# Kernel optimization log

Hardware: AMD Instinct MI355X
Metric: run time of the kernel (lower is better)

## Reference

```python
import jax, jax.numpy as jnp
import numpy as np

QUERY_SIZE = 512
KEY_SIZE = 512
VALUE_SIZE = 512
HIDDEN = 128


def setup_inputs() -> dict:
    key = jax.random.key(0)
    ks = jax.random.split(key, 9)
    b, t_q, t_k = 8, 128, 512
    query = jax.random.normal(ks[0], (b, t_q, QUERY_SIZE), dtype=jnp.float32)
    keys = jax.random.normal(ks[1], (b, t_k, KEY_SIZE), dtype=jnp.float32)
    values = jax.random.normal(ks[2], (b, t_k, VALUE_SIZE), dtype=jnp.float32)
    # torch nn.Linear init ~ U(-1/sqrt(fan_in), 1/sqrt(fan_in)); scale-matched normals are fine
    sq = 1.0 / np.sqrt(QUERY_SIZE)
    sk = 1.0 / np.sqrt(KEY_SIZE)
    sh = 1.0 / np.sqrt(HIDDEN)
    Wq = jax.random.uniform(ks[3], (HIDDEN, QUERY_SIZE), jnp.float32, -sq, sq)
    bq = jax.random.uniform(ks[4], (HIDDEN,), jnp.float32, -sq, sq)
    Wk = jax.random.uniform(ks[5], (HIDDEN, KEY_SIZE), jnp.float32, -sk, sk)
    bk = jax.random.uniform(ks[6], (HIDDEN,), jnp.float32, -sk, sk)
    Wo = jax.random.uniform(ks[7], (1, HIDDEN), jnp.float32, -sh, sh)
    bo = jax.random.uniform(ks[8], (1,), jnp.float32, -sh, sh)
    return {"query": query, "keys": keys, "values": values,
            "Wq": Wq, "bq": bq, "Wk": Wk, "bk": bk, "Wo": Wo, "bo": bo}


def reference(query, keys, values, Wq, bq, Wk, bk, Wo, bo):
    # Bahdanau additive attention: att_ij = Wo @ tanh(Wq q_i + Wk k_j + bq + bk) + bo
    # Project once per position (mathematically identical to the expanded per-pair Linear).
    q_proj = jnp.einsum('bqn,hn->bqh', query, Wq) + bq          # b x t_q x h
    k_proj = jnp.einsum('bkn,hn->bkh', keys, Wk) + bk           # b x t_k x h
    hid = jnp.tanh(q_proj[:, :, None, :] + k_proj[:, None, :, :])  # b x t_q x t_k x h
    scores = jnp.einsum('bqkh,h->bqk', hid, Wo[0]) + bo[0]       # b x t_q x t_k
    attn = jax.nn.softmax(scores, axis=2)
    context = jnp.einsum('bqk,bkv->bqv', attn, values)           # b x t_q x n_v
    return context, attn
```

## Files before the change

### kernel.cpp

```cpp
#include <hip/hip_runtime.h>


#define B_    8
#define TQ_   128
#define TK_   512
#define NIN_  512
#define H_    128
#define NV_   512
#define NQR   (B_*TQ_)
#define NROWS (NQR + B_*TK_)
#define CTXN  (B_*TQ_*NV_)

#define C2_   2.8853900817779268f
#define L2E_  1.4426950408889634f

__device__ __forceinline__ float fexp2(float x){ return __builtin_amdgcn_exp2f(x); }
__device__ __forceinline__ float frcp (float x){ return __builtin_amdgcn_rcpf(x); }

__global__ __launch_bounds__(256, 5) void proj_kernel(
        const float* __restrict__ query, const float* __restrict__ keys,
        const float* __restrict__ Wq, const float* __restrict__ Wk,
        float* __restrict__ psum, int kper) {
    __shared__ float at[32][18];
    __shared__ float wt[32][132];
    const int tid = threadIdx.x;
    const int r0  = blockIdx.x * 16;
    const float* in; const float* W;
    if (r0 < NQR) { in = query + (size_t)r0 * NIN_;         W = Wq; }
    else          { in = keys  + (size_t)(r0 - NQR) * NIN_; W = Wk; }

    const int r2 = (tid >> 5) * 2;
    const int h4 = (tid & 31) * 4;
    const int ar  = tid >> 4;
    const int ak2 = (tid & 15) * 2;
    const int wr  = tid >> 3;
    const int wkq = (tid & 7) * 4;
    const int kb0 = blockIdx.y * kper;
    const int nc  = kper >> 5;

    const float* pA  = in + (size_t)ar * NIN_ + kb0 + ak2;
    const float* pW0 = W + (size_t)(wr     ) * NIN_ + kb0 + wkq;
    const float* pW1 = W + (size_t)(wr + 32) * NIN_ + kb0 + wkq;
    const float* pW2 = W + (size_t)(wr + 64) * NIN_ + kb0 + wkq;
    const float* pW3 = W + (size_t)(wr + 96) * NIN_ + kb0 + wkq;

    float2 af = *(const float2*)pA;
    float4 w0 = *(const float4*)pW0, w1 = *(const float4*)pW1;
    float4 w2 = *(const float4*)pW2, w3 = *(const float4*)pW3;

    float acc[2][4] = {{0.f,0.f,0.f,0.f},{0.f,0.f,0.f,0.f}};

    for (int c = 0; c < nc; ++c) {
        __syncthreads();
        at[ak2+0][ar] = af.x; at[ak2+1][ar] = af.y;
        wt[wkq+0][wr   ] = w0.x; wt[wkq+1][wr   ] = w0.y;
        wt[wkq+2][wr   ] = w0.z; wt[wkq+3][wr   ] = w0.w;
        wt[wkq+0][wr+32] = w1.x; wt[wkq+1][wr+32] = w1.y;
        wt[wkq+2][wr+32] = w1.z; wt[wkq+3][wr+32] = w1.w;
        wt[wkq+0][wr+64] = w2.x; wt[wkq+1][wr+64] = w2.y;
        wt[wkq+2][wr+64] = w2.z; wt[wkq+3][wr+64] = w2.w;
        wt[wkq+0][wr+96] = w3.x; wt[wkq+1][wr+96] = w3.y;
        wt[wkq+2][wr+96] = w3.z; wt[wkq+3][wr+96] = w3.w;
        __syncthreads();
        if (c + 1 < nc) {
            pA += 32; pW0 += 32; pW1 += 32; pW2 += 32; pW3 += 32;
            af = *(const float2*)pA;
            w0 = *(const float4*)pW0; w1 = *(const float4*)pW1;
            w2 = *(const float4*)pW2; w3 = *(const float4*)pW3;
        }
#pragma unroll 8
        for (int kk = 0; kk < 32; ++kk) {
            const float2 a = *(const float2*)&at[kk][r2];
            const float4 w = *(const float4*)&wt[kk][h4];
            acc[0][0] = fmaf(a.x, w.x, acc[0][0]);
            acc[0][1] = fmaf(a.x, w.y, acc[0][1]);
            acc[0][2] = fmaf(a.x, w.z, acc[0][2]);
            acc[0][3] = fmaf(a.x, w.w, acc[0][3]);
            acc[1][0] = fmaf(a.y, w.x, acc[1][0]);
            acc[1][1] = fmaf(a.y, w.y, acc[1][1]);
            acc[1][2] = fmaf(a.y, w.z, acc[1][2]);
            acc[1][3] = fmaf(a.y, w.w, acc[1][3]);
        }
    }

    float* op = psum + ((size_t)blockIdx.y * NROWS + r0) * H_;
#pragma unroll
    for (int i = 0; i < 2; ++i) {
        float4 o = {acc[i][0], acc[i][1], acc[i][2], acc[i][3]};
        *(float4*)&op[(size_t)(r2 + i) * H_ + h4] = o;
    }
}

__global__ __launch_bounds__(256, 4) void reduceP_kernel(
        const float* __restrict__ psum, const float* __restrict__ bq,
        const float* __restrict__ bk, float* __restrict__ qe,
        float* __restrict__ keT) {
    __shared__ float lt[128][17];
    const int tid = threadIdx.x;
    const int r0  = blockIdx.x * 16;
    const bool isq = (r0 < NQR);
    const float* bias = isq ? bq : bk;

#pragma unroll
    for (int p = 0; p < 2; ++p) {
        const int j = tid + p * 256;
        const int row = j >> 5, hq = (j & 31) * 4;
        float4 s = *(const float4*)&bias[hq];
#pragma unroll
        for (int sp = 0; sp < 4; ++sp) {
            const float4 v = *(const float4*)
                &psum[((size_t)sp * NROWS + r0 + row) * H_ + hq];
            s.x += v.x; s.y += v.y; s.z += v.z; s.w += v.w;
        }
        float4 e = {fexp2(s.x * C2_), fexp2(s.y * C2_),
                    fexp2(s.z * C2_), fexp2(s.w * C2_)};
        if (isq) {
            *(float4*)&qe[(size_t)(r0 + row) * H_ + hq] = e;
        } else {
            lt[hq + 0][row] = e.x; lt[hq + 1][row] = e.y;
            lt[hq + 2][row] = e.z; lt[hq + 3][row] = e.w;
        }
    }
    if (!isq) {
        __syncthreads();
        const int b  = (r0 - NQR) >> 9;
        const int k0 = (r0 - NQR) & 511;
#pragma unroll
        for (int p = 0; p < 2; ++p) {
            const int j = tid + p * 256;
            const int h = j >> 2, kq = (j & 3) * 4;
            float4 o = {lt[h][kq], lt[h][kq + 1], lt[h][kq + 2], lt[h][kq + 3]};
            *(float4*)&keT[((size_t)b * H_ + h) * TK_ + k0 + kq] = o;
        }
    }
}

__global__ __launch_bounds__(256, 4) void scores_kernel(
        const float* __restrict__ qe, const float* __restrict__ keT,
        const float* __restrict__ Wo, const float* __restrict__ bo,
        float* __restrict__ out_attn) {
    __shared__ float qs[2][H_];
    __shared__ float w2[H_];
    __shared__ float sc[2][TK_];

    const int tid = threadIdx.x;
    const int b   = blockIdx.y;
    const int q0  = blockIdx.x * 2;
    const int lane = tid & 63;

    qs[tid >> 7][tid & 127] =
        qe[(size_t)(b * TQ_ + q0 + (tid >> 7)) * H_ + (tid & 127)];
    if (tid < H_) w2[tid] = Wo[tid] * -2.0f;
    __syncthreads();

    float sw = w2[lane] + w2[lane + 64];
#pragma unroll
    for (int m = 1; m < 64; m <<= 1) sw += __shfl_xor(sw, m);
    const float sbase = bo[0] - 0.5f * sw;

    const int k4 = (tid & 127) * 4;
    const int qi = tid >> 7;
    const float* pk = keT + (size_t)b * H_ * TK_ + k4;
    float a0 = 0.f, a1 = 0.f, a2 = 0.f, a3 = 0.f;
#pragma unroll 4
    for (int h = 0; h < H_; ++h) {
        const float4 ek = *(const float4*)pk;
        pk += TK_;
        const float qv = qs[qi][h];
        const float wv = w2[h];
        a0 = fmaf(wv, frcp(fmaf(qv, ek.x, 1.f)), a0);
        a1 = fmaf(wv, frcp(fmaf(qv, ek.y, 1.f)), a1);
        a2 = fmaf(wv, frcp(fmaf(qv, ek.z, 1.f)), a2);
        a3 = fmaf(wv, frcp(fmaf(qv, ek.w, 1.f)), a3);
    }
    float4 sv = {a0 + sbase, a1 + sbase, a2 + sbase, a3 + sbase};
    *(float4*)&sc[qi][k4] = sv;
    __syncthreads();

    const int w = tid >> 6;
    if (w < 2) {
        float4 sA = *(const float4*)&sc[w][lane * 8];
        float4 sB = *(const float4*)&sc[w][lane * 8 + 4];
        float m = fmaxf(fmaxf(fmaxf(sA.x, sA.y), fmaxf(sA.z, sA.w)),
                        fmaxf(fmaxf(sB.x, sB.y), fmaxf(sB.z, sB.w)));
#pragma unroll
        for (int mk = 1; mk < 64; mk <<= 1) m = fmaxf(m, __shfl_xor(m, mk));
        float4 eA, eB;
        eA.x = fexp2((sA.x - m) * L2E_); eA.y = fexp2((sA.y - m) * L2E_);
        eA.z = fexp2((sA.z - m) * L2E_); eA.w = fexp2((sA.w - m) * L2E_);
        eB.x = fexp2((sB.x - m) * L2E_); eB.y = fexp2((sB.y - m) * L2E_);
        eB.z = fexp2((sB.z - m) * L2E_); eB.w = fexp2((sB.w - m) * L2E_);
        float s = eA.x + eA.y + eA.z + eA.w + eB.x + eB.y + eB.z + eB.w;
#pragma unroll
        for (int mk = 1; mk < 64; mk <<= 1) s += __shfl_xor(s, mk);
        const float inv = frcp(s);
        eA.x *= inv; eA.y *= inv; eA.z *= inv; eA.w *= inv;
        eB.x *= inv; eB.y *= inv; eB.z *= inv; eB.w *= inv;
        float4* op = (float4*)&out_attn[(size_t)(b * TQ_ + q0 + w) * TK_ + lane * 8];
        op[0] = eA; op[1] = eB;
    }
}

__global__ __launch_bounds__(128, 4) void context_kernel(
        const float* __restrict__ attn, const float* __restrict__ values,
        float* __restrict__ psumC) {
    __shared__ float at[32][18];
    __shared__ float vt[32][68];

    const int tid = threadIdx.x;
    const int r0  = blockIdx.x * 16;
    const int b   = r0 >> 7;
    const int v0  = blockIdx.y * 64;
    const int kb0 = blockIdx.z * 128;

    const int q2 = (tid >> 4) * 2;
    const int v4 = (tid & 15) * 4;
    const int ar  = tid >> 3;
    const int akq = (tid & 7) * 4;
    const int vr  = tid >> 4;
    const int vq  = (tid & 15) * 4;

    const float* pAt = attn + (size_t)(r0 + ar) * TK_ + kb0 + akq;
    const float* pV0 = values + (size_t)(b * TK_ + kb0 + vr     ) * NV_ + v0 + vq;
    const float* pV1 = values + (size_t)(b * TK_ + kb0 + vr +  8) * NV_ + v0 + vq;
    const float* pV2 = values + (size_t)(b * TK_ + kb0 + vr + 16) * NV_ + v0 + vq;
    const float* pV3 = values + (size_t)(b * TK_ + kb0 + vr + 24) * NV_ + v0 + vq;

    float4 af  = *(const float4*)pAt;
    float4 vf0 = *(const float4*)pV0;
    float4 vf1 = *(const float4*)pV1;
    float4 vf2 = *(const float4*)pV2;
    float4 vf3 = *(const float4*)pV3;

    float acc[2][4] = {{0.f,0.f,0.f,0.f},{0.f,0.f,0.f,0.f}};

    for (int c = 0; c < 4; ++c) {
        __syncthreads();
        at[akq+0][ar] = af.x; at[akq+1][ar] = af.y;
        at[akq+2][ar] = af.z; at[akq+3][ar] = af.w;
        *(float4*)&vt[vr     ][vq] = vf0;
        *(float4*)&vt[vr +  8][vq] = vf1;
        *(float4*)&vt[vr + 16][vq] = vf2;
        *(float4*)&vt[vr + 24][vq] = vf3;
        __syncthreads();
        if (c + 1 < 4) {
            pAt += 32; pV0 += 32 * NV_; pV1 += 32 * NV_;
            pV2 += 32 * NV_; pV3 += 32 * NV_;
            af  = *(const float4*)pAt;
            vf0 = *(const float4*)pV0; vf1 = *(const float4*)pV1;
            vf2 = *(const float4*)pV2; vf3 = *(const float4*)pV3;
        }
#pragma unroll 8
        for (int kk = 0; kk < 32; ++kk) {
            const float2 a = *(const float2*)&at[kk][q2];
            const float4 v = *(const float4*)&vt[kk][v4];
            acc[0][0] = fmaf(a.x, v.x, acc[0][0]);
            acc[0][1] = fmaf(a.x, v.y, acc[0][1]);
            acc[0][2] = fmaf(a.x, v.z, acc[0][2]);
            acc[0][3] = fmaf(a.x, v.w, acc[0][3]);
            acc[1][0] = fmaf(a.y, v.x, acc[1][0]);
            acc[1][1] = fmaf(a.y, v.y, acc[1][1]);
            acc[1][2] = fmaf(a.y, v.z, acc[1][2]);
            acc[1][3] = fmaf(a.y, v.w, acc[1][3]);
        }
    }

    float* op = psumC + (size_t)blockIdx.z * CTXN + (size_t)r0 * NV_ + v0;
#pragma unroll
    for (int i = 0; i < 2; ++i) {
        float4 o = {acc[i][0], acc[i][1], acc[i][2], acc[i][3]};
        *(float4*)&op[(size_t)(q2 + i) * NV_ + v4] = o;
    }
}

__global__ __launch_bounds__(256, 4) void reduceC_kernel(
        const float* __restrict__ psumC, float* __restrict__ outc) {
    const size_t i = ((size_t)blockIdx.x * 256 + threadIdx.x) * 4;
    float4 s = *(const float4*)&psumC[i];
#pragma unroll
    for (int z = 1; z < 4; ++z) {
        float4 v = *(const float4*)&psumC[(size_t)z * CTXN + i];
        s.x += v.x; s.y += v.y; s.z += v.z; s.w += v.w;
    }
    *(float4*)&outc[i] = s;
}

extern "C" void kernel_launch(void* const* d_in, const int* in_sizes, int n_in,
                              void* d_out, int out_size, void* d_ws, size_t ws_size,
                              hipStream_t stream) {
    const float* query  = (const float*)d_in[0];
    const float* keys   = (const float*)d_in[1];
    const float* values = (const float*)d_in[2];
    const float* Wq     = (const float*)d_in[3];
    const float* bq     = (const float*)d_in[4];
    const float* Wk     = (const float*)d_in[5];
    const float* bk     = (const float*)d_in[6];
    const float* Wo     = (const float*)d_in[7];
    const float* bo     = (const float*)d_in[8];

    float* out_ctx  = (float*)d_out;
    float* out_attn = out_ctx + B_ * TQ_ * NV_;
    float* pout  = (float*)d_ws;
    float* qe    = pout;
    float* keT   = pout + (size_t)NQR * H_;
    float* psumP = pout + (size_t)NROWS * H_;
    float* psumC = psumP + (size_t)4 * NROWS * H_;

    proj_kernel<<<dim3(NROWS / 16, 4), 256, 0, stream>>>(
        query, keys, Wq, Wk, psumP, NIN_ / 4);
    reduceP_kernel<<<NROWS / 16, 256, 0, stream>>>(psumP, bq, bk, qe, keT);
    scores_kernel<<<dim3(TQ_ / 2, B_), 256, 0, stream>>>(qe, keT, Wo, bo, out_attn);
    context_kernel<<<dim3(NQR / 16, NV_ / 64, 4), 128, 0, stream>>>(
        out_attn, values, psumC);
    reduceC_kernel<<<CTXN / 1024, 256, 0, stream>>>(psumC, out_ctx);
}
```

Baseline: 60.62 us.

## Fuse projection reduction into proj kernel and deepen context split-K

Drops the split-K of the projection GEMM, so each block computes the full 512-long dot product and applies bias, exp and the key transpose in place, which removes the reduceP kernel and its partial-sum traffic. Shared memory is reused through a union for the transpose buffer. Separately, the context GEMM split-K factor goes from 4 to 8 (64 keys per block) for more parallelism, at the cost of more partial sums for reduceC to read. The projection grid is now 4x smaller, so fewer blocks are available to hide latency.

```diff
diff --git a/kernel.cpp b/kernel.cpp
--- a/kernel.cpp
+++ b/kernel.cpp
@@ -10,6 +10,7 @@
 #define NQR   (B_*TQ_)
 #define NROWS (NQR + B_*TK_)
 #define CTXN  (B_*TQ_*NV_)
+#define ZSPL  8
 
 #define C2_   2.8853900817779268f
 #define L2E_  1.4426950408889634f
@@ -17,17 +18,23 @@
 __device__ __forceinline__ float fexp2(float x){ return __builtin_amdgcn_exp2f(x); }
 __device__ __forceinline__ float frcp (float x){ return __builtin_amdgcn_rcpf(x); }
 
-__global__ __launch_bounds__(256, 5) void proj_kernel(
+union PSmem {
+    struct { float at[32][18]; float wt[32][132]; } m;
+    float lt[128][17];
+};
+
+__global__ __launch_bounds__(256, 4) void projE_kernel(
         const float* __restrict__ query, const float* __restrict__ keys,
         const float* __restrict__ Wq, const float* __restrict__ Wk,
-        float* __restrict__ psum, int kper) {
-    __shared__ float at[32][18];
-    __shared__ float wt[32][132];
+        const float* __restrict__ bq, const float* __restrict__ bk,
+        float* __restrict__ qe, float* __restrict__ keT) {
+    __shared__ PSmem sm;
     const int tid = threadIdx.x;
     const int r0  = blockIdx.x * 16;
-    const float* in; const float* W;
-    if (r0 < NQR) { in = query + (size_t)r0 * NIN_;         W = Wq; }
-    else          { in = keys  + (size_t)(r0 - NQR) * NIN_; W = Wk; }
+    const bool isq = (r0 < NQR);
+    const float* in; const float* W; const float* bias;
+    if (isq) { in = query + (size_t)r0 * NIN_;         W = Wq; bias = bq; }
+    else     { in = keys  + (size_t)(r0 - NQR) * NIN_; W = Wk; bias = bk; }
 
     const int r2 = (tid >> 5) * 2;
     const int h4 = (tid & 31) * 4;
@@ -35,14 +42,12 @@
     const int ak2 = (tid & 15) * 2;
     const int wr  = tid >> 3;
     const int wkq = (tid & 7) * 4;
-    const int kb0 = blockIdx.y * kper;
-    const int nc  = kper >> 5;
-
-    const float* pA  = in + (size_t)ar * NIN_ + kb0 + ak2;
-    const float* pW0 = W + (size_t)(wr     ) * NIN_ + kb0 + wkq;
-    const float* pW1 = W + (size_t)(wr + 32) * NIN_ + kb0 + wkq;
-    const float* pW2 = W + (size_t)(wr + 64) * NIN_ + kb0 + wkq;
-    const float* pW3 = W + (size_t)(wr + 96) * NIN_ + kb0 + wkq;
+
+    const float* pA  = in + (size_t)ar * NIN_ + ak2;
+    const float* pW0 = W + (size_t)(wr     ) * NIN_ + wkq;
+    const float* pW1 = W + (size_t)(wr + 32) * NIN_ + wkq;
+    const float* pW2 = W + (size_t)(wr + 64) * NIN_ + wkq;
+    const float* pW3 = W + (size_t)(wr + 96) * NIN_ + wkq;
 
     float2 af = *(const float2*)pA;
     float4 w0 = *(const float4*)pW0, w1 = *(const float4*)pW1;
@@ -50,19 +55,19 @@
 
     float acc[2][4] = {{0.f,0.f,0.f,0.f},{0.f,0.f,0.f,0.f}};
 
-    for (int c = 0; c < nc; ++c) {
-        __syncthreads();
-        at[ak2+0][ar] = af.x; at[ak2+1][ar] = af.y;
-        wt[wkq+0][wr   ] = w0.x; wt[wkq+1][wr   ] = w0.y;
-        wt[wkq+2][wr   ] = w0.z; wt[wkq+3][wr   ] = w0.w;
-        wt[wkq+0][wr+32] = w1.x; wt[wkq+1][wr+32] = w1.y;
-        wt[wkq+2][wr+32] = w1.z; wt[wkq+3][wr+32] = w1.w;
-        wt[wkq+0][wr+64] = w2.x; wt[wkq+1][wr+64] = w2.y;
-        wt[wkq+2][wr+64] = w2.z; wt[wkq+3][wr+64] = w2.w;
-        wt[wkq+0][wr+96] = w3.x; wt[wkq+1][wr+96] = w3.y;
-        wt[wkq+2][wr+96] = w3.z; wt[wkq+3][wr+96] = w3.w;
-        __syncthreads();
-        if (c + 1 < nc) {
+    for (int c = 0; c < 16; ++c) {
+        __syncthreads();
+        sm.m.at[ak2+0][ar] = af.x; sm.m.at[ak2+1][ar] = af.y;
+        sm.m.wt[wkq+0][wr   ] = w0.x; sm.m.wt[wkq+1][wr   ] = w0.y;
+        sm.m.wt[wkq+2][wr   ] = w0.z; sm.m.wt[wkq+3][wr   ] = w0.w;
+        sm.m.wt[wkq+0][wr+32] = w1.x; sm.m.wt[wkq+1][wr+32] = w1.y;
+        sm.m.wt[wkq+2][wr+32] = w1.z; sm.m.wt[wkq+3][wr+32] = w1.w;
+        sm.m.wt[wkq+0][wr+64] = w2.x; sm.m.wt[wkq+1][wr+64] = w2.y;
+        sm.m.wt[wkq+2][wr+64] = w2.z; sm.m.wt[wkq+3][wr+64] = w2.w;
+        sm.m.wt[wkq+0][wr+96] = w3.x; sm.m.wt[wkq+1][wr+96] = w3.y;
+        sm.m.wt[wkq+2][wr+96] = w3.z; sm.m.wt[wkq+3][wr+96] = w3.w;
+        __syncthreads();
+        if (c + 1 < 16) {
             pA += 32; pW0 += 32; pW1 += 32; pW2 += 32; pW3 += 32;
             af = *(const float2*)pA;
             w0 = *(const float4*)pW0; w1 = *(const float4*)pW1;
@@ -70,8 +75,8 @@
         }
 #pragma unroll 8
         for (int kk = 0; kk < 32; ++kk) {
-            const float2 a = *(const float2*)&at[kk][r2];
-            const float4 w = *(const float4*)&wt[kk][h4];
+            const float2 a = *(const float2*)&sm.m.at[kk][r2];
+            const float4 w = *(const float4*)&sm.m.wt[kk][h4];
             acc[0][0] = fmaf(a.x, w.x, acc[0][0]);
             acc[0][1] = fmaf(a.x, w.y, acc[0][1]);
             acc[0][2] = fmaf(a.x, w.z, acc[0][2]);
@@ -83,45 +88,30 @@
         }
     }
 
-    float* op = psum + ((size_t)blockIdx.y * NROWS + r0) * H_;
+    const float4 bv = *(const float4*)&bias[h4];
+    float e[2][4];
 #pragma unroll
     for (int i = 0; i < 2; ++i) {
-        float4 o = {acc[i][0], acc[i][1], acc[i][2], acc[i][3]};
-        *(float4*)&op[(size_t)(r2 + i) * H_ + h4] = o;
-    }
-}
-
-__global__ __launch_bounds__(256, 4) void reduceP_kernel(
-        const float* __restrict__ psum, const float* __restrict__ bq,
-        const float* __restrict__ bk, float* __restrict__ qe,
-        float* __restrict__ keT) {
-    __shared__ float lt[128][17];
-    const int tid = threadIdx.x;
-    const int r0  = blockIdx.x * 16;
-    const bool isq = (r0 < NQR);
-    const float* bias = isq ? bq : bk;
-
-#pragma unroll
-    for (int p = 0; p < 2; ++p) {
-        const int j = tid + p * 256;
-        const int row = j >> 5, hq = (j & 31) * 4;
-        float4 s = *(const float4*)&bias[hq];
-#pragma unroll
-        for (int sp = 0; sp < 4; ++sp) {
-            const float4 v = *(const float4*)
-                &psum[((size_t)sp * NROWS + r0 + row) * H_ + hq];
-            s.x += v.x; s.y += v.y; s.z += v.z; s.w += v.w;
-        }
-        float4 e = {fexp2(s.x * C2_), fexp2(s.y * C2_),
-                    fexp2(s.z * C2_), fexp2(s.w * C2_)};
-        if (isq) {
-            *(float4*)&qe[(size_t)(r0 + row) * H_ + hq] = e;
-        } else {
-            lt[hq + 0][row] = e.x; lt[hq + 1][row] = e.y;
-            lt[hq + 2][row] = e.z; lt[hq + 3][row] = e.w;
-        }
-    }
-    if (!isq) {
+        e[i][0] = fexp2((acc[i][0] + bv.x) * C2_);
+        e[i][1] = fexp2((acc[i][1] + bv.y) * C2_);
+        e[i][2] = fexp2((acc[i][2] + bv.z) * C2_);
+        e[i][3] = fexp2((acc[i][3] + bv.w) * C2_);
+    }
+    if (isq) {
+#pragma unroll
+        for (int i = 0; i < 2; ++i) {
+            float4 o = {e[i][0], e[i][1], e[i][2], e[i][3]};
+            *(float4*)&qe[(size_t)(r0 + r2 + i) * H_ + h4] = o;
+        }
+    } else {
+        __syncthreads();
+#pragma unroll
+        for (int i = 0; i < 2; ++i) {
+            sm.lt[h4 + 0][r2 + i] = e[i][0];
+            sm.lt[h4 + 1][r2 + i] = e[i][1];
+            sm.lt[h4 + 2][r2 + i] = e[i][2];
+            sm.lt[h4 + 3][r2 + i] = e[i][3];
+        }
         __syncthreads();
         const int b  = (r0 - NQR) >> 9;
         const int k0 = (r0 - NQR) & 511;
@@ -129,7 +119,8 @@
         for (int p = 0; p < 2; ++p) {
             const int j = tid + p * 256;
             const int h = j >> 2, kq = (j & 3) * 4;
-            float4 o = {lt[h][kq], lt[h][kq + 1], lt[h][kq + 2], lt[h][kq + 3]};
+            float4 o = {sm.lt[h][kq], sm.lt[h][kq+1],
+                        sm.lt[h][kq+2], sm.lt[h][kq+3]};
             *(float4*)&keT[((size_t)b * H_ + h) * TK_ + k0 + kq] = o;
         }
     }
@@ -201,7 +192,7 @@
     }
 }
 
-__global__ __launch_bounds__(128, 4) void context_kernel(
+__global__ __launch_bounds__(128, 8) void context_kernel(
         const float* __restrict__ attn, const float* __restrict__ values,
         float* __restrict__ psumC) {
     __shared__ float at[32][18];
@@ -211,7 +202,7 @@
     const int r0  = blockIdx.x * 16;
     const int b   = r0 >> 7;
     const int v0  = blockIdx.y * 64;
-    const int kb0 = blockIdx.z * 128;
+    const int kb0 = blockIdx.z * 64;
 
     const int q2 = (tid >> 4) * 2;
     const int v4 = (tid & 15) * 4;
@@ -234,7 +225,7 @@
 
     float acc[2][4] = {{0.f,0.f,0.f,0.f},{0.f,0.f,0.f,0.f}};
 
-    for (int c = 0; c < 4; ++c) {
+    for (int c = 0; c < 2; ++c) {
         __syncthreads();
         at[akq+0][ar] = af.x; at[akq+1][ar] = af.y;
         at[akq+2][ar] = af.z; at[akq+3][ar] = af.w;
@@ -243,7 +234,7 @@
         *(float4*)&vt[vr + 16][vq] = vf2;
         *(float4*)&vt[vr + 24][vq] = vf3;
         __syncthreads();
-        if (c + 1 < 4) {
+        if (c + 1 < 2) {
             pAt += 32; pV0 += 32 * NV_; pV1 += 32 * NV_;
             pV2 += 32 * NV_; pV3 += 32 * NV_;
             af  = *(const float4*)pAt;
@@ -278,7 +269,7 @@
     const size_t i = ((size_t)blockIdx.x * 256 + threadIdx.x) * 4;
     float4 s = *(const float4*)&psumC[i];
 #pragma unroll
-    for (int z = 1; z < 4; ++z) {
+    for (int z = 1; z < ZSPL; ++z) {
         float4 v = *(const float4*)&psumC[(size_t)z * CTXN + i];
         s.x += v.x; s.y += v.y; s.z += v.z; s.w += v.w;
     }
@@ -300,17 +291,14 @@
 
     float* out_ctx  = (float*)d_out;
     float* out_attn = out_ctx + B_ * TQ_ * NV_;
-    float* pout  = (float*)d_ws;
-    float* qe    = pout;
-    float* keT   = pout + (size_t)NQR * H_;
-    float* psumP = pout + (size_t)NROWS * H_;
-    float* psumC = psumP + (size_t)4 * NROWS * H_;
-
-    proj_kernel<<<dim3(NROWS / 16, 4), 256, 0, stream>>>(
-        query, keys, Wq, Wk, psumP, NIN_ / 4);
-    reduceP_kernel<<<NROWS / 16, 256, 0, stream>>>(psumP, bq, bk, qe, keT);
+    float* qe    = (float*)d_ws;
+    float* keT   = qe + (size_t)NQR * H_;
+    float* psumC = keT + (size_t)B_ * H_ * TK_;
+
+    projE_kernel<<<NROWS / 16, 256, 0, stream>>>(
+        query, keys, Wq, Wk, bq, bk, qe, keT);
     scores_kernel<<<dim3(TQ_ / 2, B_), 256, 0, stream>>>(qe, keT, Wo, bo, out_attn);
-    context_kernel<<<dim3(NQR / 16, NV_ / 64, 4), 128, 0, stream>>>(
+    context_kernel<<<dim3(NQR / 16, NV_ / 64, ZSPL), 128, 0, stream>>>(
         out_attn, values, psumC);
     reduceC_kernel<<<CTXN / 1024, 256, 0, stream>>>(psumC, out_ctx);
 }
```

After: 114.9 us. +89.6%, slower.
